# Optimization experiments

Measured on AMD Instinct MI355X. Metric: run time of the kernel, lower is better.

The kernel has to match this reference:

```python
import jax, jax.numpy as jnp
import numpy as np

B, S, H, F, G = 8, 2048, 1024, 4096, 128
EPS = 1e-5


def setup_inputs() -> dict:
    key = jax.random.key(0)
    ks = jax.random.split(key, 8)
    x = jax.random.normal(ks[0], (B, S, H), dtype=jnp.float32)
    ln_gamma = jnp.ones((H,), jnp.float32)
    ln_beta = jnp.zeros((H,), jnp.float32)
    # int8-style quantized weights stored as int32 in [0, 256) with zero-point 128
    fc1_q = jax.random.randint(ks[1], (H, F), 0, 256, dtype=jnp.int32)
    fc2_q = jax.random.randint(ks[2], (F, H), 0, 256, dtype=jnp.int32)
    # per-group scales (one scale per 128 rows of K, per output column)
    fc1_scales = jax.random.uniform(ks[3], (H // G, F), jnp.float32) * 0.02 + 0.001
    fc2_scales = jax.random.uniform(ks[4], (F // G, H), jnp.float32) * 0.02 + 0.001
    fc1_bias = jax.random.normal(ks[5], (F,), jnp.float32) * 0.02
    fc2_bias = jax.random.normal(ks[6], (H,), jnp.float32) * 0.02
    return {"x": x, "ln_gamma": ln_gamma, "ln_beta": ln_beta,
            "fc1_q": fc1_q, "fc1_scales": fc1_scales, "fc1_bias": fc1_bias,
            "fc2_q": fc2_q, "fc2_scales": fc2_scales, "fc2_bias": fc2_bias}


def _dequant(q, scales, g):
    # q: [K, N] int, scales: [K//g, N]; zero-point 128 symmetric int8 scheme
    K, N = q.shape
    w = (q.astype(jnp.float32) - 128.0).reshape(K // g, g, N) * scales[:, None, :]
    return w.reshape(K, N)


def reference(x, ln_gamma, ln_beta, fc1_q, fc1_scales, fc1_bias, fc2_q, fc2_scales, fc2_bias):
    residual = x
    # LayerNorm over last dim
    mu = jnp.mean(x, axis=-1, keepdims=True)
    var = jnp.mean(jnp.square(x - mu), axis=-1, keepdims=True)
    h = (x - mu) * jax.lax.rsqrt(var + EPS) * ln_gamma + ln_beta
    hf = h.reshape(-1, H)                       # [B*S, H]
    w1 = _dequant(fc1_q, fc1_scales, G)         # [H, F]
    y = hf @ w1 + fc1_bias                      # [B*S, F]
    y = jax.nn.silu(y)                          # dropout is identity at inference
    w2 = _dequant(fc2_q, fc2_scales, G)         # [F, H]
    z = y @ w2 + fc2_bias                       # [B*S, H]
    return residual + 0.5 * z.reshape(residual.shape)
```

## Files before the change

### kernel.cpp

```cpp
#include <hip/hip_runtime.h>
#include <hip/hip_bf16.h>

#define HH 1024
#define FF 4096
#define MTOT (8 * 2048)

typedef __attribute__((ext_vector_type(4))) float f32x4;
typedef __attribute__((ext_vector_type(8))) short bf16x8;

__device__ inline void async_load16(const void* g, void* l) {
    __builtin_amdgcn_global_load_lds(
        (const __attribute__((address_space(1))) unsigned int*)g,
        (__attribute__((address_space(3))) unsigned int*)l, 16, 0, 0);
}
__device__ inline unsigned lds_off(void* p) {
    return (unsigned)(size_t)(__attribute__((address_space(3))) char*)p;
}
template<int OFF>
__device__ inline bf16x8 dsr(unsigned addr) {
    bf16x8 r;
    asm volatile("ds_read_b128 %0, %1 offset:%2" : "=v"(r) : "v"(addr), "n"(OFF));
    return r;
}
#define SBAR()  __builtin_amdgcn_s_barrier()
#define LGKM0() do { asm volatile("s_waitcnt lgkmcnt(0)"); \
                     __builtin_amdgcn_sched_barrier(0); } while (0)
#define WAIT_VM8() asm volatile("s_waitcnt vmcnt(8)")
#define WAIT_VM0() asm volatile("s_waitcnt vmcnt(0)")

template<int BUF, int MH>
__device__ inline void ldA(bf16x8 (&d)[4][2], unsigned vA0, unsigned vA1) {
    constexpr int B = BUF * 32768 + MH * 8192;
    d[0][0] = dsr<B + 0>(vA0);     d[0][1] = dsr<B + 0>(vA1);
    d[1][0] = dsr<B + 2048>(vA0);  d[1][1] = dsr<B + 2048>(vA1);
    d[2][0] = dsr<B + 4096>(vA0);  d[2][1] = dsr<B + 4096>(vA1);
    d[3][0] = dsr<B + 6144>(vA0);  d[3][1] = dsr<B + 6144>(vA1);
}
template<int BUF, int NH>
__device__ inline void ldB(bf16x8 (&d)[2][2], unsigned vB0, unsigned vB1) {
    constexpr int B = BUF * 32768 + NH * 4096;
    d[0][0] = dsr<B + 0>(vB0);     d[0][1] = dsr<B + 0>(vB1);
    d[1][0] = dsr<B + 2048>(vB0);  d[1][1] = dsr<B + 2048>(vB1);
}

__global__ void dequant_t_kernel(const int* __restrict__ q,
                                 const float* __restrict__ scales,
                                 __hip_bfloat16* __restrict__ wt,
                                 int K, int N)
{
    __shared__ float tile[32][33];
    const int n0 = blockIdx.x * 32, k0 = blockIdx.y * 32;
    const int tx = threadIdx.x, ty = threadIdx.y;
#pragma unroll
    for (int i = 0; i < 32; i += 8) {
        int k = k0 + ty + i, n = n0 + tx;
        float s = scales[(size_t)(k >> 7) * N + n];
        tile[ty + i][tx] = (float)(q[(size_t)k * N + n] - 128) * s;
    }
    __syncthreads();
#pragma unroll
    for (int i = 0; i < 32; i += 8) {
        int n = n0 + ty + i, k = k0 + tx;
        wt[(size_t)n * K + k] = __float2bfloat16(tile[tx][ty + i]);
    }
}

__global__ __launch_bounds__(256)
void ln_kernel(const float* __restrict__ x, const float* __restrict__ gamma,
               const float* __restrict__ beta, __hip_bfloat16* __restrict__ hf,
               int m0)
{
    const int row = m0 + blockIdx.x;
    const float4 v = ((const float4*)(x + (size_t)row * HH))[threadIdx.x];
    float s  = v.x + v.y + v.z + v.w;
    float ss = v.x * v.x + v.y * v.y + v.z * v.z + v.w * v.w;
#pragma unroll
    for (int o = 32; o > 0; o >>= 1) { s += __shfl_down(s, o); ss += __shfl_down(ss, o); }
    __shared__ float red[8];
    const int wid = threadIdx.x >> 6, lane = threadIdx.x & 63;
    if (lane == 0) { red[wid] = s; red[4 + wid] = ss; }
    __syncthreads();
    if (threadIdx.x == 0) {
        red[0] = red[0] + red[1] + red[2] + red[3];
        red[4] = red[4] + red[5] + red[6] + red[7];
    }
    __syncthreads();
    const float mu   = red[0] * (1.f / HH);
    const float rstd = rsqrtf(red[4] * (1.f / HH) - mu * mu + 1e-5f);
    const float4 g = ((const float4*)gamma)[threadIdx.x];
    const float4 b = ((const float4*)beta)[threadIdx.x];
    float h0 = (v.x - mu) * rstd * g.x + b.x;
    float h1 = (v.y - mu) * rstd * g.y + b.y;
    float h2 = (v.z - mu) * rstd * g.z + b.z;
    float h3 = (v.w - mu) * rstd * g.w + b.w;
    __hip_bfloat16 t0 = __float2bfloat16(h0), t1 = __float2bfloat16(h1);
    __hip_bfloat16 t2 = __float2bfloat16(h2), t3 = __float2bfloat16(h3);
    ushort4 o;
    o.x = *(unsigned short*)&t0; o.y = *(unsigned short*)&t1;
    o.z = *(unsigned short*)&t2; o.w = *(unsigned short*)&t3;
    ((ushort4*)(hf + (size_t)blockIdx.x * HH))[threadIdx.x] = o;
}

template<int EPI, int KK>
__global__ __launch_bounds__(512, 2)
void gemm256(const __hip_bfloat16* __restrict__ A,
             const __hip_bfloat16* __restrict__ Bt,
             const float* __restrict__ bias,
             const float* __restrict__ resid,
             void* __restrict__ outv,
             int N, int nbx)
{
    __shared__ __align__(16) short SM[65536];
    constexpr int NT = KK >> 6;

    const int nwg = (int)gridDim.x, b = (int)blockIdx.x;
    const int q = nwg >> 3, r = nwg & 7;
    const int xcd = b & 7, pos = b >> 3;
    const int bid = (xcd < r) ? xcd * (q + 1) + pos
                              : r * (q + 1) + (xcd - r) * q + pos;
    const int bx = bid % nbx, by = bid / nbx;
    const int rowA0 = by * 256, colB0 = bx * 256;

    const int tid = (int)threadIdx.x;
    const int lane = tid & 63, wid = tid >> 6;
    const int wr = wid >> 2, wc = wid & 3;
    const int lrow = lane & 15, kg = lane >> 4;
    const int swz = lrow & 7;

    const int srow = tid >> 3;
    const int sgs  = (tid & 7) ^ (srow & 7);
    const __hip_bfloat16* aSrc = A  + (size_t)(rowA0 + srow) * KK + sgs * 8;
    const __hip_bfloat16* bSrc = Bt + (size_t)(colB0 + srow) * KK + sgs * 8;
    short* aDst = SM + srow * 64 + (tid & 7) * 8;
    short* bDst = SM + 32768 + srow * 64 + (tid & 7) * 8;

    const unsigned asB = lds_off(SM);
    const unsigned k0off = (unsigned)((kg ^ swz) << 4);
    const unsigned k1off = (unsigned)(((4 + kg) ^ swz) << 4);
    const unsigned vA0 = asB + (unsigned)((wr * 128 + lrow) * 128) + k0off;
    const unsigned vA1 = asB + (unsigned)((wr * 128 + lrow) * 128) + k1off;
    const unsigned vB0 = asB + 65536u + (unsigned)((wc * 64 + lrow) * 128) + k0off;
    const unsigned vB1 = asB + 65536u + (unsigned)((wc * 64 + lrow) * 128) + k1off;

    auto stA = [&](int buf, int t, int half) {
        const size_t ko = (size_t)t * 64;
        short* d = aDst + buf * 16384 + half * 8192;
        const __hip_bfloat16* s0 = aSrc + (size_t)(half * 128) * KK + ko;
        async_load16(s0, d);
        async_load16(s0 + (size_t)64 * KK, d + 4096);
    };
    auto stB = [&](int buf, int t, int half) {
        const size_t ko = (size_t)t * 64;
        short* d = bDst + buf * 16384 + half * 8192;
        const __hip_bfloat16* s0 = bSrc + (size_t)(half * 128) * KK + ko;
        async_load16(s0, d);
        async_load16(s0 + (size_t)64 * KK, d + 4096);
    };

    f32x4 acc[8][4] = {};
    auto mf = [&](const bf16x8 (&a)[4][2], const bf16x8 (&bb)[2][2], int mh, int nh) {
        __builtin_amdgcn_s_setprio(1);
#pragma unroll
        for (int ks = 0; ks < 2; ++ks)
#pragma unroll
            for (int m2 = 0; m2 < 4; ++m2)
#pragma unroll
                for (int n2 = 0; n2 < 2; ++n2)
                    acc[mh * 4 + m2][nh * 2 + n2] =
                        __builtin_amdgcn_mfma_f32_16x16x32_bf16(
                            a[m2][ks], bb[n2][ks], acc[mh * 4 + m2][nh * 2 + n2], 0, 0, 0);
        __builtin_amdgcn_s_setprio(0);
    };

    stA(0, 0, 0); stA(0, 0, 1); stB(0, 0, 0); stB(0, 0, 1);
    stA(1, 1, 0); stB(1, 1, 0); stA(1, 1, 1); stB(1, 1, 1);
    WAIT_VM8();
    SBAR();

    bf16x8 a0[4][2], a1[4][2], b0[2][2], b1[2][2];
    const int NI = NT >> 1;
    for (int i = 0; i < NI; ++i) {
        const int c = 2 * i, n = 2 * i + 1;
        const bool last = (i == NI - 1);
        ldA<0, 0>(a0, vA0, vA1); ldB<0, 0>(b0, vB0, vB1);
        SBAR(); LGKM0();
        mf(a0, b0, 0, 0);
        SBAR();
        ldB<0, 1>(b1, vB0, vB1);
        SBAR(); LGKM0();
        mf(a0, b1, 0, 1);
        SBAR();
        ldA<0, 1>(a1, vA0, vA1);
        if (!last) { stA(0, c + 2, 0); stB(0, c + 2, 0); }
        SBAR(); LGKM0();
        mf(a1, b0, 1, 0);
        SBAR();
        if (!last) { stA(0, c + 2, 1); stB(0, c + 2, 1); WAIT_VM8(); }
        else       { WAIT_VM0(); }
        SBAR();
        mf(a1, b1, 1, 1);
        SBAR();
        ldA<1, 0>(a0, vA0, vA1); ldB<1, 0>(b0, vB0, vB1);
        SBAR(); LGKM0();
        mf(a0, b0, 0, 0);
        SBAR();
        ldB<1, 1>(b1, vB0, vB1);
        SBAR(); LGKM0();
        mf(a0, b1, 0, 1);
        SBAR();
        ldA<1, 1>(a1, vA0, vA1);
        if (!last) { stA(1, n + 2, 0); stB(1, n + 2, 0); }
        SBAR(); LGKM0();
        mf(a1, b0, 1, 0);
        SBAR();
        if (!last) { stA(1, n + 2, 1); stB(1, n + 2, 1); WAIT_VM8(); }
        SBAR();
        mf(a1, b1, 1, 1);
        SBAR();
    }
    WAIT_VM0();

    __syncthreads();

    if (EPI == 0) {
        short* smh = SM;
#pragma unroll
        for (int ni = 0; ni < 4; ++ni) {
            const int col = wc * 64 + ni * 16 + lrow;
            const float bv = bias[colB0 + col];
#pragma unroll
            for (int mi = 0; mi < 8; ++mi) {
#pragma unroll
                for (int j = 0; j < 4; ++j) {
                    const int rowl = wr * 128 + mi * 16 + kg * 4 + j;
                    const float v = acc[mi][ni][j] + bv;
                    const float sv = v / (1.f + __expf(-v));
                    const __hip_bfloat16 hb = __float2bfloat16(sv);
                    const int sidx = rowl * 256 + ((((col >> 3) ^ (rowl & 7)) << 3) | (col & 7));
                    smh[sidx] = *(const short*)&hb;
                }
            }
        }
        __syncthreads();
        __hip_bfloat16* yp = (__hip_bfloat16*)outv;
#pragma unroll
        for (int p = 0; p < 16; ++p) {
            const int idx = p * 512 + tid;
            const int rowl = idx >> 5, s = idx & 31;
            const bf16x8 v8 = *(const bf16x8*)&smh[rowl * 256 + ((s ^ (rowl & 7)) << 3)];
            *(bf16x8*)(yp + (size_t)(rowA0 + rowl) * N + colB0 + s * 8) = v8;
        }
    } else {
        float* smf = (float*)SM;
        float* op = (float*)outv;
#pragma unroll
        for (int h = 0; h < 2; ++h) {
            if (wr == h) {
#pragma unroll
                for (int ni = 0; ni < 4; ++ni) {
                    const int col = wc * 64 + ni * 16 + lrow;
                    const float bv = bias[colB0 + col];
#pragma unroll
                    for (int mi = 0; mi < 8; ++mi) {
#pragma unroll
                        for (int j = 0; j < 4; ++j) {
                            const int rowl = mi * 16 + kg * 4 + j;
                            const float v = acc[mi][ni][j] + bv;
                            const int fidx = rowl * 256 +
                                ((((col >> 2) ^ (rowl & 7)) << 2) | (col & 3));
                            smf[fidx] = v;
                        }
                    }
                }
            }
            __syncthreads();
#pragma unroll
            for (int p = 0; p < 16; ++p) {
                const int idx = p * 512 + tid;
                const int rowl = idx >> 6, s = idx & 63;
                const f32x4 v4 = *(const f32x4*)&smf[rowl * 256 + ((s ^ (rowl & 7)) << 2)];
                const size_t g = (size_t)(rowA0 + h * 128 + rowl) * N + colB0 + s * 4;
                const float4 rv = *(const float4*)&resid[g];
                float4 o4;
                o4.x = rv.x + 0.5f * v4[0];
                o4.y = rv.y + 0.5f * v4[1];
                o4.z = rv.z + 0.5f * v4[2];
                o4.w = rv.w + 0.5f * v4[3];
                *(float4*)&op[g] = o4;
            }
            __syncthreads();
        }
    }
}

extern "C" void kernel_launch(void* const* d_in, const int* in_sizes, int n_in,
                              void* d_out, int out_size, void* d_ws, size_t ws_size,
                              hipStream_t stream)
{
    const float* x      = (const float*)d_in[0];
    const float* gamma  = (const float*)d_in[1];
    const float* beta   = (const float*)d_in[2];
    const int*   fc1_q  = (const int*)d_in[3];
    const float* fc1_s  = (const float*)d_in[4];
    const float* fc1_b  = (const float*)d_in[5];
    const int*   fc2_q  = (const int*)d_in[6];
    const float* fc2_s  = (const float*)d_in[7];
    const float* fc2_b  = (const float*)d_in[8];
    float* out = (float*)d_out;

    char* ws = (char*)d_ws;
    __hip_bfloat16* w1t = (__hip_bfloat16*)ws;
    __hip_bfloat16* w2t = (__hip_bfloat16*)(ws + (size_t)FF * HH * 2);
    char* dyn = ws + (size_t)2 * FF * HH * 2;
    const size_t avail = ws_size - (size_t)2 * FF * HH * 2;

    int MC = (int)(avail / ((size_t)(HH + FF) * 2));
    MC = (MC / 256) * 256;
    if (MC > MTOT) MC = MTOT;
    if (MC < 256)  MC = 256;

    __hip_bfloat16* hf_c = (__hip_bfloat16*)dyn;
    __hip_bfloat16* y_c  = (__hip_bfloat16*)(dyn + (size_t)MC * HH * 2);

    dequant_t_kernel<<<dim3(FF / 32, HH / 32), dim3(32, 8), 0, stream>>>(
        fc1_q, fc1_s, w1t, HH, FF);
    dequant_t_kernel<<<dim3(HH / 32, FF / 32), dim3(32, 8), 0, stream>>>(
        fc2_q, fc2_s, w2t, FF, HH);

    for (int m0 = 0; m0 < MTOT; m0 += MC) {
        const int mc = (MTOT - m0 < MC) ? (MTOT - m0) : MC;
        ln_kernel<<<mc, 256, 0, stream>>>(x, gamma, beta, hf_c, m0);
        gemm256<0, HH><<<dim3((FF / 256) * (mc / 256)), 512, 0, stream>>>(
            hf_c, w1t, fc1_b, nullptr, (void*)y_c, FF, FF / 256);
        gemm256<1, FF><<<dim3((HH / 256) * (mc / 256)), 512, 0, stream>>>(
            y_c, w2t, fc2_b, x + (size_t)m0 * HH, (void*)(out + (size_t)m0 * HH),
            HH, HH / 256);
    }
}
```

Measured before the change: 318.4 us.

## Restructure GEMM main loop with single-tile prefetch and staged LDS waits

Rewrites the double-buffered GEMM K-loop. The old loop kept two tiles of async global-to-LDS loads in flight and used about eight barriers per tile. The new loop issues all LDS fragment reads for a tile up front, then uses staged lgkmcnt waits so the MFMAs start as soon as their operands arrive, with one barrier per tile. The cost is a shallower global prefetch: each half-iteration waits for vmcnt(0), so global load latency must be hidden within a single tile's compute.

```diff
diff --git a/kernel.cpp b/kernel.cpp
--- a/kernel.cpp
+++ b/kernel.cpp
@@ -23,9 +23,11 @@
     return r;
 }
 #define SBAR()  __builtin_amdgcn_s_barrier()
-#define LGKM0() do { asm volatile("s_waitcnt lgkmcnt(0)"); \
-                     __builtin_amdgcn_sched_barrier(0); } while (0)
-#define WAIT_VM8() asm volatile("s_waitcnt vmcnt(8)")
+template<int N>
+__device__ inline void LGKM() {
+    asm volatile("s_waitcnt lgkmcnt(%0)" :: "n"(N));
+    __builtin_amdgcn_sched_barrier(0);
+}
 #define WAIT_VM0() asm volatile("s_waitcnt vmcnt(0)")
 
 template<int BUF, int MH>
@@ -173,52 +175,43 @@
     };
 
     stA(0, 0, 0); stA(0, 0, 1); stB(0, 0, 0); stB(0, 0, 1);
-    stA(1, 1, 0); stB(1, 1, 0); stA(1, 1, 1); stB(1, 1, 1);
-    WAIT_VM8();
+    WAIT_VM0();
     SBAR();
 
     bf16x8 a0[4][2], a1[4][2], b0[2][2], b1[2][2];
     const int NI = NT >> 1;
     for (int i = 0; i < NI; ++i) {
         const int c = 2 * i, n = 2 * i + 1;
-        const bool last = (i == NI - 1);
-        ldA<0, 0>(a0, vA0, vA1); ldB<0, 0>(b0, vB0, vB1);
-        SBAR(); LGKM0();
+        stA(1, n, 0); stA(1, n, 1); stB(1, n, 0); stB(1, n, 1);
+        ldA<0, 0>(a0, vA0, vA1);
+        ldB<0, 0>(b0, vB0, vB1);
+        ldB<0, 1>(b1, vB0, vB1);
+        ldA<0, 1>(a1, vA0, vA1);
+        LGKM<12>();
         mf(a0, b0, 0, 0);
+        LGKM<8>();
+        mf(a0, b1, 0, 1);
+        LGKM<0>();
+        mf(a1, b0, 1, 0);
+        mf(a1, b1, 1, 1);
+        WAIT_VM0();
         SBAR();
-        ldB<0, 1>(b1, vB0, vB1);
-        SBAR(); LGKM0();
+        if (i < NI - 1) { stA(0, c + 2, 0); stA(0, c + 2, 1);
+                          stB(0, c + 2, 0); stB(0, c + 2, 1); }
+        ldA<1, 0>(a0, vA0, vA1);
+        ldB<1, 0>(b0, vB0, vB1);
+        ldB<1, 1>(b1, vB0, vB1);
+        ldA<1, 1>(a1, vA0, vA1);
+        LGKM<12>();
+        mf(a0, b0, 0, 0);
+        LGKM<8>();
         mf(a0, b1, 0, 1);
+        LGKM<0>();
+        mf(a1, b0, 1, 0);
+        mf(a1, b1, 1, 1);
+        WAIT_VM0();
         SBAR();
-        ldA<0, 1>(a1, vA0, vA1);
-        if (!last) { stA(0, c + 2, 0); stB(0, c + 2, 0); }
-        SBAR(); LGKM0();
-        mf(a1, b0, 1, 0);
-        SBAR();
-        if (!last) { stA(0, c + 2, 1); stB(0, c + 2, 1); WAIT_VM8(); }
-        else       { WAIT_VM0(); }
-        SBAR();
-        mf(a1, b1, 1, 1);
-        SBAR();
-        ldA<1, 0>(a0, vA0, vA1); ldB<1, 0>(b0, vB0, vB1);
-        SBAR(); LGKM0();
-        mf(a0, b0, 0, 0);
-        SBAR();
-        ldB<1, 1>(b1, vB0, vB1);
-        SBAR(); LGKM0();
-        mf(a0, b1, 0, 1);
-        SBAR();
-        ldA<1, 1>(a1, vA0, vA1);
-        if (!last) { stA(1, n + 2, 0); stB(1, n + 2, 0); }
-        SBAR(); LGKM0();
-        mf(a1, b0, 1, 0);
-        SBAR();
-        if (!last) { stA(1, n + 2, 1); stB(1, n + 2, 1); WAIT_VM8(); }
-        SBAR();
-        mf(a1, b1, 1, 1);
-        SBAR();
-    }
-    WAIT_VM0();
+    }
 
     __syncthreads();
 
```

Result: no change. 313.9 us (-1.4%).
